# Kernel optimization log

Hardware: AMD Instinct MI355X
Metric: run time of the kernel (lower is better)

Reference implementation:

```python
import jax, jax.numpy as jnp
import numpy as np

NINP, NHID, NOUT, DT = 128, 768, 128, 1.0
T, B = 256, 256


def setup_inputs() -> dict:
    key = jax.random.key(0)
    ks = jax.random.split(key, 9)
    std = 1.0 / np.sqrt(NHID)
    u = lambda k, shape: jax.random.uniform(k, shape, jnp.float32, -std, std)
    return {
        "input": jax.random.normal(ks[0], (T, B, NINP), jnp.float32),
        "W_inp": u(ks[1], (4 * NHID, NINP)),
        "b_inp": u(ks[2], (4 * NHID,)),
        "W_hid": u(ks[3], (3 * NHID, NHID)),
        "b_hid": u(ks[4], (3 * NHID,)),
        "W_z": u(ks[5], (NHID, NHID)),
        "b_z": u(ks[6], (NHID,)),
        "W_cls": jax.random.normal(ks[7], (NOUT, NHID), jnp.float32) * np.sqrt(2.0 / NHID),
        "b_cls": u(ks[8], (NOUT,)),
    }


def reference(input, W_inp, b_inp, W_hid, b_hid, W_z, b_z, W_cls, b_cls):
    # Precompute input projections for all timesteps: [T, B, 4*NHID]
    inp_proj = jnp.einsum('tbi,hi->tbh', input, W_inp) + b_inp

    def step(carry, xi):
        y, z = carry
        hid = y @ W_hid.T + b_hid                     # [B, 3*NHID]
        i_dt1, i_dt2, i_z, i_y = jnp.split(xi, 4, axis=1)
        h_dt1, h_dt2, h_y = jnp.split(hid, 3, axis=1)
        ms_dt_bar = DT * jax.nn.sigmoid(i_dt1 + h_dt1)
        ms_dt = DT * jax.nn.sigmoid(i_dt2 + h_dt2)
        z = (1.0 - ms_dt) * z + ms_dt * jnp.tanh(i_y + h_y)
        y = (1.0 - ms_dt_bar) * y + ms_dt_bar * jnp.tanh(z @ W_z.T + b_z + i_z)
        return (y, z), None

    y0 = jnp.zeros((input.shape[1], NHID), input.dtype)
    z0 = jnp.zeros_like(y0)
    (y, z), _ = jax.lax.scan(step, (y0, z0), inp_proj)
    return y @ W_cls.T + b_cls
```

## Files before the change

### kernel.cpp

```cpp
#include <hip/hip_runtime.h>
#include <stdint.h>


#define NINP 128
#define NHID 768
#define NOUT 128
#define T_STEPS 256
#define BATCH 256

#define NGRP 8
#define CBLK 24
#define NBLK 192
#define NTHR 256

#define NHTILES 144
#define SBUF 196608
#define WZ_ELEMS (1152 * 512)
#define WI_ELEMS (768 * 512)
#define XF_ELEMS (256 * 2 * 4 * 16 * 512)

typedef short bf16x8 __attribute__((ext_vector_type(8)));
typedef float f32x4 __attribute__((ext_vector_type(4)));

__device__ __forceinline__ unsigned short f2b(float f) {
  union { float f; unsigned u; } x; x.f = f;
  return (unsigned short)((x.u + 0x7fffu + ((x.u >> 16) & 1u)) >> 16);
}
__device__ __forceinline__ float b2f(unsigned short h) {
  union { unsigned u; float f; } x; x.u = ((unsigned)h) << 16; return x.f;
}
__device__ __forceinline__ float fsig(float x) { return 1.0f / (1.0f + __expf(-x)); }
__device__ __forceinline__ float ftanh(float x) {
  float e = __expf(2.0f * x);
  return 1.0f - 2.0f / (e + 1.0f);
}

#define MFMA16(a, b, c) __builtin_amdgcn_mfma_f32_16x16x32_bf16(a, b, c, 0, 0, 0)

#define AL32(p) __hip_atomic_load((const unsigned*)(p), __ATOMIC_RELAXED, __HIP_MEMORY_SCOPE_AGENT)
#define AS32(p, v) __hip_atomic_store((unsigned*)(p), (v), __ATOMIC_RELAXED, __HIP_MEMORY_SCOPE_AGENT)
#define AS16(p, v) __hip_atomic_store((unsigned short*)(p), (v), __ATOMIC_RELAXED, __HIP_MEMORY_SCOPE_AGENT)

__device__ __forceinline__ void uld16(bf16x8* dst, const unsigned short* addr) {
  asm volatile("global_load_dwordx4 %0, %1, off sc0 sc1" : "=v"(*dst) : "v"(addr));
}
__device__ __forceinline__ void cld16(bf16x8* dst, const unsigned short* addr) {
  asm volatile("global_load_dwordx4 %0, %1, off" : "=v"(*dst) : "v"(addr));
}
#define WAITV(N) do { \
  asm volatile("s_waitcnt vmcnt(" #N ")" ::: "memory"); \
  __builtin_amdgcn_sched_barrier(0); } while (0)

__device__ __forceinline__ void split8(const float* p, bf16x8* hi, bf16x8* lo) {
  union { bf16x8 v; unsigned short s[8]; } H, L;
#pragma unroll
  for (int e = 0; e < 8; ++e) {
    float v = p[e];
    unsigned short h = f2b(v);
    H.s[e] = h;
    L.s[e] = f2b(v - b2f(h));
  }
  *hi = H.v; *lo = L.v;
}

__global__ __launch_bounds__(256) void conv_w(
    const float* __restrict__ W_z, const float* __restrict__ W_inp,
    unsigned short* __restrict__ Wz, unsigned short* __restrict__ Wi) {
  int idx = blockIdx.x * 256 + threadIdx.x;
  int t = idx >> 9, r = idx & 511;
  int ll = r >> 3, e = r & 7;
  int col16 = ll & 15;
  int kk = ((ll >> 4) * 8) + e;
  if (t < 1152) {
    int kt = t % 24, ct = (t / 24) & 1, c = t / 48;
    Wz[idx] = f2b(W_z[(size_t)(c * 32 + ct * 16 + col16) * NHID + kt * 32 + kk]);
  } else {
    int u = t - 1152;
    int xkt = u & 3, ct = (u >> 2) & 1, seg = (u >> 3) & 3, c = u >> 5;
    Wi[(size_t)u * 512 + r] =
        f2b(W_inp[(size_t)(seg * NHID + c * 32 + ct * 16 + col16) * NINP + xkt * 32 + kk]);
  }
}

__global__ __launch_bounds__(256) void xprep(
    const float* __restrict__ x, unsigned short* __restrict__ XF) {
  int gid = blockIdx.x * 256 + threadIdx.x;
  int lane = gid & 63;
  int rtx = (gid >> 6) & 15;
  int xkt = (gid >> 10) & 3;
  int t = gid >> 12;
  int kg = lane >> 4, r16 = lane & 15;
  int row = rtx * 16 + r16;
  bf16x8 hi, lo;
  split8(x + ((size_t)t * BATCH + row) * NINP + xkt * 32 + kg * 8, &hi, &lo);
  size_t lo_off = (size_t)kg * 128 + r16 * 8;
  *(bf16x8*)(XF + ((((size_t)t * 2 + 0) * 4 + xkt) * 16 + rtx) * 512 + lo_off) = hi;
  *(bf16x8*)(XF + ((((size_t)t * 2 + 1) * 4 + xkt) * 16 + rtx) * 512 + lo_off) = lo;
}

__global__ __launch_bounds__(NTHR, 1) void lem_kernel(
    const float* __restrict__ b_inp,
    const float* __restrict__ W_hid,
    const float* __restrict__ b_hid,
    const float* __restrict__ b_z,
    const float* __restrict__ W_cls,
    const float* __restrict__ b_cls,
    float* __restrict__ out,
    unsigned short* __restrict__ Y,
    unsigned short* __restrict__ Z,
    unsigned* __restrict__ flags,
    const unsigned short* __restrict__ Wz,
    const unsigned short* __restrict__ Wi,
    const unsigned short* __restrict__ XF)
{
  __shared__ unsigned short wlds[NHTILES * 512];
  __shared__ float red[128 * 24];

  const int tid = threadIdx.x;
  const int l   = tid & 63;
  const int w   = tid >> 6;
  const int rtl = w & 1;
  const int kh  = w >> 1;
  const int g   = blockIdx.x / CBLK;
  const int c   = blockIdx.x % CBLK;
  const int colbase = c * 32;
  const int lc  = l & 15;
  const int kg8 = (l >> 4) * 8;
  const int laneoff = (l >> 4) * 128 + lc * 8;
  const int rtg = g * 2 + rtl;
  const int r16b = (l >> 4) * 4;

  for (int idx = tid; idx < NHTILES * 512; idx += NTHR) {
    int t = idx >> 9;
    int r = idx & 511;
    int ll = r >> 3, e = r & 7;
    int col16 = ll & 15;
    int kk = ((ll >> 4) * 8) + e;
    int kt = t % 24, cs = t / 24;
    int ct = cs / 3, seg = cs % 3;
    wlds[idx] = f2b(W_hid[(size_t)(seg * NHID + colbase + ct * 16 + col16) * NHID + kt * 32 + kk]);
  }

#define LDSB(t) (*(const bf16x8*)&wlds[((t) << 9) + (l << 3)])

  float c1[2], c2[2], cy[2], cz[2];
  unsigned short *zs[2], *ys[2];
#pragma unroll
  for (int ct = 0; ct < 2; ++ct) {
    int col = colbase + ct * 16 + lc;
    c1[ct] = b_inp[col] + b_hid[col];
    c2[ct] = b_inp[NHID + col] + b_hid[NHID + col];
    cy[ct] = b_inp[3 * NHID + col] + b_hid[2 * NHID + col];
    cz[ct] = b_inp[2 * NHID + col] + b_z[col];
    int kts = col >> 5, kgs = (col >> 3) & 3, es = col & 7;
    zs[ct] = Z + ((kts * 16 + rtg) * 4 + kgs) * 128 + es;
    ys[ct] = Y + ((kts * 16 + rtg) * 4 + kgs) * 128 + es;
  }
  unsigned* gfA = flags + g * 128;
  unsigned* gfB = gfA + 64;
  const int khb = kh * 12;

  bf16x8 wifA[3][2][2];
  bf16x8 wiB[2][2];
#pragma unroll
  for (int hseg = 0; hseg < 3; ++hseg) {
    int wseg = (hseg == 2) ? 3 : hseg;
#pragma unroll
    for (int ct = 0; ct < 2; ++ct)
#pragma unroll
      for (int xk2 = 0; xk2 < 2; ++xk2)
        cld16(&wifA[hseg][ct][xk2],
              Wi + (size_t)((((c * 4 + wseg) * 2 + ct) * 4) + (kh * 2 + xk2)) * 512 + l * 8);
  }
#pragma unroll
  for (int ct = 0; ct < 2; ++ct)
#pragma unroll
    for (int xk2 = 0; xk2 < 2; ++xk2)
      cld16(&wiB[ct][xk2],
            Wi + (size_t)((((c * 4 + 2) * 2 + ct) * 4) + (kh * 2 + xk2)) * 512 + l * 8);

  bf16x8 xa[4];
#define ISSUE_XA(sidx) do { \
    cld16(&xa[0], XF + ((((size_t)(sidx) * 2 + 0) * 4 + (kh * 2 + 0)) * 16 + rtg) * 512 + laneoff); \
    cld16(&xa[1], XF + ((((size_t)(sidx) * 2 + 1) * 4 + (kh * 2 + 0)) * 16 + rtg) * 512 + laneoff); \
    cld16(&xa[2], XF + ((((size_t)(sidx) * 2 + 0) * 4 + (kh * 2 + 1)) * 16 + rtg) * 512 + laneoff); \
    cld16(&xa[3], XF + ((((size_t)(sidx) * 2 + 1) * 4 + (kh * 2 + 1)) * 16 + rtg) * 512 + laneoff); } while (0)

  ISSUE_XA(0);
  WAITV(0);
  __syncthreads();

  f32x4 yloc[2], zloc[2], msb[2];
#pragma unroll
  for (int ct = 0; ct < 2; ++ct) { yloc[ct] = f32x4{0,0,0,0}; zloc[ct] = f32x4{0,0,0,0}; }

  float* rp = red + ((size_t)rtl * 64 + l) * 24;

  bf16x8 ybufs[6][2];
  bf16x8 zbuf[6];
  bf16x8 wzf[6][2];
  const unsigned short* wzb0 = Wz + (size_t)((c * 2 + 0) * 24) * 512 + l * 8;
  const unsigned short* wzb1 = Wz + (size_t)((c * 2 + 1) * 24) * 512 + l * 8;

#define ISSUE_Y(slot, j) do { \
    int kt_ = khb + 2 * (j); \
    uld16(&ybufs[slot][0], Y + (size_t)(kt_ * 16 + rtg) * 512 + laneoff); \
    uld16(&ybufs[slot][1], Y + (size_t)((kt_ + 1) * 16 + rtg) * 512 + laneoff); } while (0)

#define ISSUE_Z(slot, j) do { \
    int kt_ = khb + (j); \
    uld16(&zbuf[slot], Z + (size_t)(kt_ * 16 + rtg) * 512 + laneoff); \
    cld16(&wzf[slot][0], wzb0 + (size_t)kt_ * 512); \
    cld16(&wzf[slot][1], wzb1 + (size_t)kt_ * 512); } while (0)

  for (int s = 0; s < T_STEPS; ++s) {
    f32x4 h[3][2];
#pragma unroll
    for (int sg = 0; sg < 3; ++sg)
#pragma unroll
      for (int ct = 0; ct < 2; ++ct) h[sg][ct] = f32x4{0,0,0,0};

    ISSUE_Y(0, 0); ISSUE_Y(1, 1); ISSUE_Y(2, 2);
    WAITV(6);
#pragma unroll
    for (int xk2 = 0; xk2 < 2; ++xk2)
#pragma unroll
      for (int sg = 0; sg < 3; ++sg)
#pragma unroll
        for (int ct = 0; ct < 2; ++ct) {
          h[sg][ct] = MFMA16(xa[xk2 * 2 + 0], wifA[sg][ct][xk2], h[sg][ct]);
          h[sg][ct] = MFMA16(xa[xk2 * 2 + 1], wifA[sg][ct][xk2], h[sg][ct]);
        }
#pragma unroll
    for (int j = 0; j < 6; ++j) {
      if (j < 3) ISSUE_Y(j + 3, j + 3);
      if (j < 3) { WAITV(6); } else if (j == 3) { WAITV(4); }
      else if (j == 4) { WAITV(2); } else { WAITV(0); }
#pragma unroll
      for (int i2 = 0; i2 < 2; ++i2) {
        int ktp = khb + 2 * j + i2;
        bf16x8 a = ybufs[j][i2];
#pragma unroll
        for (int ct = 0; ct < 2; ++ct)
#pragma unroll
          for (int sg = 0; sg < 3; ++sg)
            h[sg][ct] = MFMA16(a, LDSB((ct * 3 + sg) * 24 + ktp), h[sg][ct]);
      }
    }
    if (kh == 1) {
#pragma unroll
      for (int sg = 0; sg < 3; ++sg)
#pragma unroll
        for (int ct = 0; ct < 2; ++ct)
          *(f32x4*)(rp + (sg * 2 + ct) * 4) = h[sg][ct];
    }
    __syncthreads();
    if (kh == 0) {
#pragma unroll
      for (int sg = 0; sg < 3; ++sg)
#pragma unroll
        for (int ct = 0; ct < 2; ++ct)
          h[sg][ct] += *(const f32x4*)(rp + (sg * 2 + ct) * 4);
#pragma unroll
      for (int ct = 0; ct < 2; ++ct)
#pragma unroll
        for (int i = 0; i < 4; ++i) {
          float a1 = fsig(h[0][ct][i] + c1[ct]);
          float a2 = fsig(h[1][ct][i] + c2[ct]);
          float gg = ftanh(h[2][ct][i] + cy[ct]);
          float zn = (1.0f - a2) * zloc[ct][i] + a2 * gg;
          zloc[ct][i] = zn;
          msb[ct][i] = a1;
          AS16(zs[ct] + (r16b + i) * 8, f2b(zn));
        }
    }
    __syncthreads();
    if (tid == 0) AS32(&gfA[c], (unsigned)(s + 1));
    if (w == 0) {
      const unsigned* fp = gfA + (l < CBLK ? l : 0);
      while (true) {
        unsigned v = AL32(fp);
        if (__all((l >= CBLK) || (v >= (unsigned)(s + 1)))) break;
        __builtin_amdgcn_s_sleep(1);
      }
    }
    __syncthreads();

    f32x4 az[2];
    az[0] = f32x4{0,0,0,0}; az[1] = f32x4{0,0,0,0};
    ISSUE_Z(0, 0); ISSUE_Z(1, 1); ISSUE_Z(2, 2); ISSUE_Z(3, 3); ISSUE_Z(4, 4);
#pragma unroll
    for (int xk2 = 0; xk2 < 2; ++xk2)
#pragma unroll
      for (int ct = 0; ct < 2; ++ct) {
        az[ct] = MFMA16(xa[xk2 * 2 + 0], wiB[ct][xk2], az[ct]);
        az[ct] = MFMA16(xa[xk2 * 2 + 1], wiB[ct][xk2], az[ct]);
      }
#pragma unroll
    for (int j = 0; j < 12; ++j) {
      if (j < 7) ISSUE_Z((j + 5) % 6, j + 5);
      if (j < 7) { WAITV(15); } else if (j == 7) { WAITV(12); }
      else if (j == 8) { WAITV(9); } else if (j == 9) { WAITV(6); }
      else if (j == 10) { WAITV(3); } else { WAITV(0); }
      const int sl = j % 6;
      az[0] = MFMA16(zbuf[sl], wzf[sl][0], az[0]);
      az[1] = MFMA16(zbuf[sl], wzf[sl][1], az[1]);
    }
    if (kh == 1) {
      *(f32x4*)(rp + 0) = az[0];
      *(f32x4*)(rp + 4) = az[1];
    }
    __syncthreads();
    if (kh == 0) {
      az[0] += *(const f32x4*)(rp + 0);
      az[1] += *(const f32x4*)(rp + 4);
#pragma unroll
      for (int ct = 0; ct < 2; ++ct)
#pragma unroll
        for (int i = 0; i < 4; ++i) {
          float tt = ftanh(az[ct][i] + cz[ct]);
          float yn = (1.0f - msb[ct][i]) * yloc[ct][i] + msb[ct][i] * tt;
          yloc[ct][i] = yn;
          AS16(ys[ct] + (r16b + i) * 8, f2b(yn));
        }
    }
    __syncthreads();
    if (tid == 0) AS32(&gfB[c], (unsigned)(s + 1));
    if (s + 1 < T_STEPS) ISSUE_XA(s + 1);
    if (w == 0) {
      const unsigned* fp = gfB + (l < CBLK ? l : 0);
      while (true) {
        unsigned v = AL32(fp);
        if (__all((l >= CBLK) || (v >= (unsigned)(s + 1)))) break;
        __builtin_amdgcn_s_sleep(1);
      }
    }
    __syncthreads();
  }

  if (c < 8) {
    const int ocb = c * 16;
    f32x4 ao{0, 0, 0, 0};
    bf16x8 yb[12];
#pragma unroll
    for (int j = 0; j < 12; ++j)
      uld16(&yb[j], Y + (size_t)((khb + j) * 16 + rtg) * 512 + laneoff);
    WAITV(0);
#pragma unroll
    for (int j = 0; j < 12; ++j) {
      int kt = khb + j;
      bf16x8 bh, bl;
      split8(W_cls + (size_t)(ocb + lc) * NHID + kt * 32 + kg8, &bh, &bl);
      ao = MFMA16(yb[j], bh, ao);
      ao = MFMA16(yb[j], bl, ao);
    }
    if (kh == 1) *(f32x4*)(rp + 0) = ao;
    __syncthreads();
    if (kh == 0) {
      ao += *(const f32x4*)(rp + 0);
      float bc = b_cls[ocb + lc];
#pragma unroll
      for (int i = 0; i < 4; ++i)
        out[(size_t)(g * 32 + rtl * 16 + r16b + i) * NOUT + ocb + lc] = ao[i] + bc;
    }
  }
}

extern "C" void kernel_launch(void* const* d_in, const int* in_sizes, int n_in,
                              void* d_out, int out_size, void* d_ws, size_t ws_size,
                              hipStream_t stream) {
  (void)in_sizes; (void)n_in; (void)out_size; (void)ws_size;
  const float* x     = (const float*)d_in[0];
  const float* W_inp = (const float*)d_in[1];
  const float* b_inp = (const float*)d_in[2];
  const float* W_hid = (const float*)d_in[3];
  const float* b_hid = (const float*)d_in[4];
  const float* W_z   = (const float*)d_in[5];
  const float* b_z   = (const float*)d_in[6];
  const float* W_cls = (const float*)d_in[7];
  const float* b_cls = (const float*)d_in[8];

  unsigned short* Y = (unsigned short*)d_ws;
  unsigned short* Z = Y + SBUF;
  unsigned* flags = (unsigned*)(Z + SBUF);
  unsigned short* Wz = (unsigned short*)(flags + NGRP * 128);
  unsigned short* Wi = Wz + WZ_ELEMS;
  unsigned short* XF = Wi + WI_ELEMS;

  hipMemsetAsync(d_ws, 0, 2 * SBUF * sizeof(unsigned short) + NGRP * 128 * sizeof(unsigned), stream);

  conv_w<<<dim3(3840), dim3(256), 0, stream>>>(W_z, W_inp, Wz, Wi);
  xprep<<<dim3(4096), dim3(256), 0, stream>>>(x, XF);

  lem_kernel<<<dim3(NBLK), dim3(NTHR), 0, stream>>>(
      b_inp, W_hid, b_hid, b_z, W_cls, b_cls,
      (float*)d_out, Y, Z, flags, Wz, Wi, XF);
}
```

Before: 2.115 ms.

## Stage Z/Y state through LDS for 16-byte stores and prefetch all Y loads

Instead of each thread issuing eight scattered 16-bit atomic stores of the new z and y values to global memory, the values are first written into a small LDS transpose buffer. Each lane then reads back one contiguous 8-element chunk and writes it with a single 16-byte cache-bypassing store. Separately, all six Y-tile loads are issued up front rather than staggered, with the wait counts adjusted to match. This cuts the number of global store transactions on the serial recurrence's critical path, at the cost of an LDS round trip and more registers held for in-flight loads.

After: 2.066 ms. 1.02x faster.

```diff
diff --git a/kernel.cpp b/kernel.cpp
--- a/kernel.cpp
+++ b/kernel.cpp
@@ -17,7 +17,6 @@
 #define SBUF 196608
 #define WZ_ELEMS (1152 * 512)
 #define WI_ELEMS (768 * 512)
-#define XF_ELEMS (256 * 2 * 4 * 16 * 512)
 
 typedef short bf16x8 __attribute__((ext_vector_type(8)));
 typedef float f32x4 __attribute__((ext_vector_type(4)));
@@ -39,13 +38,15 @@
 
 #define AL32(p) __hip_atomic_load((const unsigned*)(p), __ATOMIC_RELAXED, __HIP_MEMORY_SCOPE_AGENT)
 #define AS32(p, v) __hip_atomic_store((unsigned*)(p), (v), __ATOMIC_RELAXED, __HIP_MEMORY_SCOPE_AGENT)
-#define AS16(p, v) __hip_atomic_store((unsigned short*)(p), (v), __ATOMIC_RELAXED, __HIP_MEMORY_SCOPE_AGENT)
 
 __device__ __forceinline__ void uld16(bf16x8* dst, const unsigned short* addr) {
   asm volatile("global_load_dwordx4 %0, %1, off sc0 sc1" : "=v"(*dst) : "v"(addr));
 }
 __device__ __forceinline__ void cld16(bf16x8* dst, const unsigned short* addr) {
   asm volatile("global_load_dwordx4 %0, %1, off" : "=v"(*dst) : "v"(addr));
+}
+__device__ __forceinline__ void ust16(unsigned short* addr, bf16x8 v) {
+  asm volatile("global_store_dwordx4 %0, %1, off sc0 sc1" :: "v"(addr), "v"(v) : "memory");
 }
 #define WAITV(N) do { \
   asm volatile("s_waitcnt vmcnt(" #N ")" ::: "memory"); \
@@ -115,6 +116,7 @@
 {
   __shared__ unsigned short wlds[NHTILES * 512];
   __shared__ float red[128 * 24];
+  __shared__ unsigned short zt[2 * 512];
 
   const int tid = threadIdx.x;
   const int l   = tid & 63;
@@ -144,7 +146,6 @@
 #define LDSB(t) (*(const bf16x8*)&wlds[((t) << 9) + (l << 3)])
 
   float c1[2], c2[2], cy[2], cz[2];
-  unsigned short *zs[2], *ys[2];
 #pragma unroll
   for (int ct = 0; ct < 2; ++ct) {
     int col = colbase + ct * 16 + lc;
@@ -152,13 +153,12 @@
     c2[ct] = b_inp[NHID + col] + b_hid[NHID + col];
     cy[ct] = b_inp[3 * NHID + col] + b_hid[2 * NHID + col];
     cz[ct] = b_inp[2 * NHID + col] + b_z[col];
-    int kts = col >> 5, kgs = (col >> 3) & 3, es = col & 7;
-    zs[ct] = Z + ((kts * 16 + rtg) * 4 + kgs) * 128 + es;
-    ys[ct] = Y + ((kts * 16 + rtg) * 4 + kgs) * 128 + es;
   }
   unsigned* gfA = flags + g * 128;
   unsigned* gfB = gfA + 64;
   const int khb = kh * 12;
+  unsigned short* Zc = Z + (size_t)(c * 16 + rtg) * 512;
+  unsigned short* Yc = Y + (size_t)(c * 16 + rtg) * 512;
 
   bf16x8 wifA[3][2][2];
   bf16x8 wiB[2][2];
@@ -194,7 +194,8 @@
 #pragma unroll
   for (int ct = 0; ct < 2; ++ct) { yloc[ct] = f32x4{0,0,0,0}; zloc[ct] = f32x4{0,0,0,0}; }
 
-  float* rp = red + ((size_t)rtl * 64 + l) * 24;
+  float* rp = red + (rtl * 64 + l) * 24;
+  unsigned short* trow = zt + rtl * 512;
 
   bf16x8 ybufs[6][2];
   bf16x8 zbuf[6];
@@ -221,7 +222,8 @@
       for (int ct = 0; ct < 2; ++ct) h[sg][ct] = f32x4{0,0,0,0};
 
     ISSUE_Y(0, 0); ISSUE_Y(1, 1); ISSUE_Y(2, 2);
-    WAITV(6);
+    ISSUE_Y(3, 3); ISSUE_Y(4, 4); ISSUE_Y(5, 5);
+    WAITV(12);
 #pragma unroll
     for (int xk2 = 0; xk2 < 2; ++xk2)
 #pragma unroll
@@ -233,8 +235,8 @@
         }
 #pragma unroll
     for (int j = 0; j < 6; ++j) {
-      if (j < 3) ISSUE_Y(j + 3, j + 3);
-      if (j < 3) { WAITV(6); } else if (j == 3) { WAITV(4); }
+      if (j == 0) { WAITV(10); } else if (j == 1) { WAITV(8); }
+      else if (j == 2) { WAITV(6); } else if (j == 3) { WAITV(4); }
       else if (j == 4) { WAITV(2); } else { WAITV(0); }
 #pragma unroll
       for (int i2 = 0; i2 < 2; ++i2) {
@@ -271,8 +273,13 @@
           float zn = (1.0f - a2) * zloc[ct][i] + a2 * gg;
           zloc[ct][i] = zn;
           msb[ct][i] = a1;
-          AS16(zs[ct] + (r16b + i) * 8, f2b(zn));
+          int jj = ct * 16 + lc;
+          trow[((jj >> 3) * 16 + r16b + i) * 8 + (jj & 7)] = f2b(zn);
         }
+      asm volatile("s_waitcnt lgkmcnt(0)" ::: "memory");
+      __builtin_amdgcn_sched_barrier(0);
+      bf16x8 zrun = *(const bf16x8*)(trow + l * 8);
+      ust16(Zc + l * 8, zrun);
     }
     __syncthreads();
     if (tid == 0) AS32(&gfA[c], (unsigned)(s + 1));
@@ -321,8 +328,13 @@
           float tt = ftanh(az[ct][i] + cz[ct]);
           float yn = (1.0f - msb[ct][i]) * yloc[ct][i] + msb[ct][i] * tt;
           yloc[ct][i] = yn;
-          AS16(ys[ct] + (r16b + i) * 8, f2b(yn));
+          int jj = ct * 16 + lc;
+          trow[((jj >> 3) * 16 + r16b + i) * 8 + (jj & 7)] = f2b(yn);
         }
+      asm volatile("s_waitcnt lgkmcnt(0)" ::: "memory");
+      __builtin_amdgcn_sched_barrier(0);
+      bf16x8 yrun = *(const bf16x8*)(trow + l * 8);
+      ust16(Yc + l * 8, yrun);
     }
     __syncthreads();
     if (tid == 0) AS32(&gfB[c], (unsigned)(s + 1));
```
